# Kernel tuning notes

Measured on AMD Instinct MI355X. Metric: run time of the kernel, lower is better.

## Reference

```python
import jax, jax.numpy as jnp
import numpy as np

LEAKY_ALPHA = 0.2  # tf.nn.leaky_relu default

B, N, F_IN, HID = 1, 8192, 512, 256


def setup_inputs() -> dict:
    key = jax.random.key(0)
    ks = jax.random.split(key, 4)
    seq = jax.random.normal(ks[0], (B, N, F_IN), dtype=jnp.float32)
    bias_mat = jnp.zeros((B, N, N), dtype=jnp.float32)  # 0 = edge present (fully connected mask)
    W = jax.random.normal(ks[1], (F_IN, HID), dtype=jnp.float32) * (1.0 / np.sqrt(F_IN))
    a1 = jax.random.normal(ks[2], (HID, 1), dtype=jnp.float32) * (1.0 / np.sqrt(HID))
    b1 = jnp.zeros((1,), dtype=jnp.float32)
    a2 = jax.random.normal(ks[3], (HID, 1), dtype=jnp.float32) * (1.0 / np.sqrt(HID))
    b2 = jnp.zeros((1,), dtype=jnp.float32)
    bias_zero = jnp.zeros((HID,), dtype=jnp.float32)
    return {"seq": seq, "bias_mat": bias_mat, "W": W, "a1": a1, "b1": b1,
            "a2": a2, "b2": b2, "bias_zero": bias_zero}


def reference(seq, bias_mat, W, a1, b1, a2, b2, bias_zero):
    # Conv1D(kernel=1, no bias) == per-node linear projection
    seq_fts = jnp.einsum('bnf,fh->bnh', seq, W)            # [B,N,H]
    f_1 = jnp.einsum('bnh,ho->bno', seq_fts, a1) + b1      # [B,N,1]
    f_2 = jnp.einsum('bnh,ho->bno', seq_fts, a2) + b2      # [B,N,1]
    logits = f_1 + jnp.swapaxes(f_2, 1, 2)                 # [B,N,N] outer-sum
    scores = jnp.where(logits > 0, logits, LEAKY_ALPHA * logits) + bias_mat
    coefs = jax.nn.softmax(scores, axis=-1)                # masked softmax over neighbors
    vals = jnp.einsum('bnm,bmh->bnh', coefs, seq_fts)      # aggregation
    ret = vals + bias_zero
    return jax.nn.elu(ret)
```

## Files before the change

kernel.cpp:

```cpp
#include <hip/hip_runtime.h>
#include <hip/hip_bf16.h>
#include <stdint.h>

#define NN 8192
#define FIN 512
#define HID 256

typedef short bf16x8 __attribute__((ext_vector_type(8)));
typedef float f32x4 __attribute__((ext_vector_type(4)));

__device__ __forceinline__ uint32_t pk2(float lo, float hi) {
  uint32_t a = __float_as_uint(lo), b = __float_as_uint(hi);
  a = (a + 0x7FFFu + ((a >> 16) & 1u)) >> 16;
  b = (b + 0x7FFFu + ((b >> 16) & 1u)) >> 16;
  return a | (b << 16);
}

#define OFF_SEQB   0u
#define OFF_WTB    8388608u
#define OFF_FTST   8650752u
#define OFF_F1     12845056u
#define OFF_F2     12877824u
#define OFF_Z      12910592u
#define OFF_F2MAX  12943360u

__global__ void k_cvt_seq(const float* __restrict__ seq, short* __restrict__ seqb) {
  int i = (blockIdx.x * 256 + threadIdx.x) * 4;
  float4 v = *(const float4*)(seq + i);
  uint2 o; o.x = pk2(v.x, v.y); o.y = pk2(v.z, v.w);
  *(uint2*)(seqb + i) = o;
}

__global__ void k_wt(const float* __restrict__ W, short* __restrict__ WTb) {
  int h = blockIdx.x;
  int t = threadIdx.x;
  int k = t * 2;
  float w0 = W[k * 256 + h], w1 = W[(k + 1) * 256 + h];
  ((uint32_t*)(WTb + h * 512))[t] = pk2(w0, w1);
}

__global__ __launch_bounds__(256) void k_proj(
    const short* __restrict__ seqb, const short* __restrict__ WTb,
    const float* __restrict__ a1, const float* __restrict__ b1,
    const float* __restrict__ a2, const float* __restrict__ b2,
    short* __restrict__ ftsP, float* __restrict__ f1g, float* __restrict__ f2g,
    uint32_t* __restrict__ f2maxenc) {
  __shared__ short At[64][72];
  __shared__ float f1a[64], f2a[64];
  const int t = threadIdx.x;
  const int l = t & 63, w = t >> 6;
  const int lr = l & 15, lg = l >> 4;
  const int R0 = blockIdx.x * 64;
  const int srow = t >> 2, scol = (t & 3) * 16;
  f32x4 acc[4][4] = {};
  if (t < 64) { f1a[t] = 0.f; f2a[t] = 0.f; }
  for (int kt = 0; kt < FIN; kt += 64) {
    uint4 s0 = *(const uint4*)(seqb + (size_t)(R0 + srow) * FIN + kt + scol);
    uint4 s1 = *(const uint4*)(seqb + (size_t)(R0 + srow) * FIN + kt + scol + 8);
    __syncthreads();
    *(uint4*)&At[srow][scol] = s0;
    *(uint4*)&At[srow][scol + 8] = s1;
    __syncthreads();
#pragma unroll
    for (int kk = 0; kk < 2; ++kk) {
      bf16x8 af[4];
#pragma unroll
      for (int mf = 0; mf < 4; ++mf)
        af[mf] = *(const bf16x8*)&At[mf * 16 + lr][kk * 32 + lg * 8];
#pragma unroll
      for (int nf = 0; nf < 4; ++nf) {
        int h = w * 64 + nf * 16 + lr;
        bf16x8 bfr = *(const bf16x8*)(WTb + h * FIN + kt + kk * 32 + lg * 8);
#pragma unroll
        for (int mf = 0; mf < 4; ++mf)
          acc[mf][nf] = __builtin_amdgcn_mfma_f32_16x16x32_bf16(af[mf], bfr, acc[mf][nf], 0, 0, 0);
      }
    }
  }
  __syncthreads();
  float a1v[4], a2v[4];
#pragma unroll
  for (int nf = 0; nf < 4; ++nf) {
    int h = w * 64 + nf * 16 + lr;
    a1v[nf] = a1[h]; a2v[nf] = a2[h];
  }
#pragma unroll
  for (int mf = 0; mf < 4; ++mf) {
    const int jo = mf * 16 + lg * 4;
    const int slot = (jo >> 3) ^ (lr & 7);
#pragma unroll
    for (int nf = 0; nf < 4; ++nf) {
      int h = w * 64 + nf * 16 + lr;
      uint2 o; o.x = pk2(acc[mf][nf][0], acc[mf][nf][1]);
      o.y = pk2(acc[mf][nf][2], acc[mf][nf][3]);
      *(uint2*)(ftsP + (size_t)blockIdx.x * 16384 + h * 64 + slot * 8 + (jo & 7)) = o;
    }
#pragma unroll
    for (int e = 0; e < 4; ++e) {
      float p1 = 0.f, p2 = 0.f;
#pragma unroll
      for (int nf = 0; nf < 4; ++nf) { p1 += acc[mf][nf][e] * a1v[nf]; p2 += acc[mf][nf][e] * a2v[nf]; }
#pragma unroll
      for (int m = 8; m >= 1; m >>= 1) { p1 += __shfl_xor(p1, m, 16); p2 += __shfl_xor(p2, m, 16); }
      if (lr == 0) {
        atomicAdd(&f1a[mf * 16 + lg * 4 + e], p1);
        atomicAdd(&f2a[mf * 16 + lg * 4 + e], p2);
      }
    }
  }
  __syncthreads();
  if (t < 64) {
    float v1 = f1a[t] + b1[0];
    float v2 = f2a[t] + b2[0];
    f1g[R0 + t] = v1; f2g[R0 + t] = v2;
    uint32_t u = __float_as_uint(v2);
    u = (u & 0x80000000u) ? ~u : (u | 0x80000000u);
    atomicMax(f2maxenc, u);
  }
}

__global__ __launch_bounds__(512, 4) void k_flash(
    const float* __restrict__ bias, const short* __restrict__ ftsP,
    const float* __restrict__ f1g, const float* __restrict__ f2g,
    const uint32_t* __restrict__ f2maxenc,
    float* __restrict__ outacc, float* __restrict__ Zg) {
  __shared__ short Vb[2][16384];
  const int t = threadIdx.x;
  const int l = t & 63, wid = t >> 6;
  const int lr = l & 15, lg = l >> 4;
  const int hh = wid & 1;
  const int rg = wid >> 1;
  const int rbase = blockIdx.x * 64 + rg * 16;
  const int rowA = rbase + lr;
  const int jbase = blockIdx.y * 2048;
  const int jt0 = jbase >> 6;
  const int NT = 32;
  const int nfb = hh * 8;

  uint32_t ue = *f2maxenc;
  float f2mx = __uint_as_float((ue & 0x80000000u) ? (ue ^ 0x80000000u) : ~ue);
  float f1v = f1g[rowA];
  float xm = f1v + f2mx;
  float mr = fmaxf(xm, 0.2f * xm);

  const float* bp = bias + (size_t)rowA * NN + jbase + lg * 8;
  const float* qp = f2g + jbase + lg * 8;

  const int s0 = lg ^ (lr & 7);
  const int s1 = s0 ^ 4;

  f32x4 acc[8] = {};
  float z = 0.f;
  float4 bb[2][2], qq[2][2];

#define STAGE(TT, BUF)                                                          \
  if ((TT) < NT) {                                                              \
    const short* gs = ftsP + (size_t)(jt0 + (TT)) * 16384 + wid * 2048 + l * 8; \
    _Pragma("unroll")                                                           \
    for (int c = 0; c < 4; ++c)                                                 \
      __builtin_amdgcn_global_load_lds(                                         \
          (const __attribute__((address_space(1))) void*)(gs + c * 512),        \
          (__attribute__((address_space(3))) void*)&Vb[(BUF)][wid * 2048 + c * 512], \
          16, 0, 0);                                                            \
  }
#define LOADB(TT)                                                               \
  if ((TT) < NT) {                                                              \
    _Pragma("unroll")                                                           \
    for (int kk = 0; kk < 2; ++kk) {                                            \
      _Pragma("unroll")                                                         \
      for (int h4 = 0; h4 < 2; ++h4) {                                          \
        bb[kk][h4] = *(const float4*)(bp + (TT) * 64 + kk * 32 + h4 * 4);       \
        qq[kk][h4] = *(const float4*)(qp + (TT) * 64 + kk * 32 + h4 * 4);       \
      }                                                                         \
    }                                                                           \
  }
#define EHALF(BBK, QQK, AOUT)                                                   \
  {                                                                             \
    float p[8];                                                                 \
    _Pragma("unroll")                                                           \
    for (int e = 0; e < 4; ++e) {                                               \
      float s = f1v + ((const float*)&QQK[0])[e];                               \
      float ls = fmaxf(s, 0.2f * s);                                            \
      p[e] = __expf(ls + ((const float*)&BBK[0])[e] - mr);                      \
    }                                                                           \
    _Pragma("unroll")                                                           \
    for (int e = 0; e < 4; ++e) {                                               \
      float s = f1v + ((const float*)&QQK[1])[e];                               \
      float ls = fmaxf(s, 0.2f * s);                                            \
      p[4 + e] = __expf(ls + ((const float*)&BBK[1])[e] - mr);                  \
    }                                                                           \
    z += ((p[0] + p[1]) + (p[2] + p[3])) + ((p[4] + p[5]) + (p[6] + p[7]));     \
    union { bf16x8 v; uint32_t u[4]; } A;                                       \
    A.u[0] = pk2(p[0], p[1]); A.u[1] = pk2(p[2], p[3]);                         \
    A.u[2] = pk2(p[4], p[5]); A.u[3] = pk2(p[6], p[7]);                         \
    AOUT = A.v;                                                                 \
  }

  STAGE(0, 0)
  STAGE(1, 1)
  LOADB(0)
  __syncthreads();

  for (int tt = 0; tt < NT; ++tt) {
    bf16x8 A0, A1;
    EHALF(bb[0], qq[0], A0)
    EHALF(bb[1], qq[1], A1)

    LOADB(tt + 1)

    {
      const int cb = tt & 1;
      const short* vr0 = &Vb[cb][lr * 64 + s0 * 8];
      const short* vr1 = &Vb[cb][lr * 64 + s1 * 8];
#pragma unroll
      for (int nf = 0; nf < 8; ++nf) {
        bf16x8 B0 = *(const bf16x8*)(vr0 + (nfb + nf) * 1024);
        acc[nf] = __builtin_amdgcn_mfma_f32_16x16x32_bf16(A0, B0, acc[nf], 0, 0, 0);
      }
#pragma unroll
      for (int nf = 0; nf < 8; ++nf) {
        bf16x8 B1 = *(const bf16x8*)(vr1 + (nfb + nf) * 1024);
        acc[nf] = __builtin_amdgcn_mfma_f32_16x16x32_bf16(A1, B1, acc[nf], 0, 0, 0);
      }
    }

    __syncthreads();
    STAGE(tt + 2, tt & 1)
  }
#undef STAGE
#undef LOADB
#undef EHALF

  z += __shfl_xor(z, 16);
  z += __shfl_xor(z, 32);
  if (hh == 0 && lg == 0) atomicAdd(&Zg[rowA], z);

#pragma unroll
  for (int nf = 0; nf < 8; ++nf) {
    int col = (nfb + nf) * 16 + lr;
#pragma unroll
    for (int e = 0; e < 4; ++e)
      atomicAdd(&outacc[(size_t)(rbase + lg * 4 + e) * HID + col], acc[nf][e]);
  }
}

__global__ void k_final(float* __restrict__ outp, const float* __restrict__ Zg,
                        const float* __restrict__ bz) {
  int i4 = (blockIdx.x * 256 + threadIdx.x) * 4;
  int row = i4 >> 8;
  int col = i4 & 255;
  float4 v = *(float4*)(outp + i4);
  float zr = 1.0f / Zg[row];
  float4 b = *(const float4*)(bz + col);
  float r[4] = {v.x * zr + b.x, v.y * zr + b.y, v.z * zr + b.z, v.w * zr + b.w};
#pragma unroll
  for (int e = 0; e < 4; ++e) r[e] = r[e] > 0.f ? r[e] : (__expf(r[e]) - 1.f);
  *(float4*)(outp + i4) = make_float4(r[0], r[1], r[2], r[3]);
}

extern "C" void kernel_launch(void* const* d_in, const int* in_sizes, int n_in,
                              void* d_out, int out_size, void* d_ws, size_t ws_size,
                              hipStream_t stream) {
  const float* seq  = (const float*)d_in[0];
  const float* bias = (const float*)d_in[1];
  const float* W    = (const float*)d_in[2];
  const float* a1   = (const float*)d_in[3];
  const float* b1   = (const float*)d_in[4];
  const float* a2   = (const float*)d_in[5];
  const float* b2   = (const float*)d_in[6];
  const float* bz   = (const float*)d_in[7];
  float* out = (float*)d_out;
  char* ws = (char*)d_ws;
  short* seqb = (short*)(ws + OFF_SEQB);
  short* WTb  = (short*)(ws + OFF_WTB);
  short* ftsP = (short*)(ws + OFF_FTST);
  float* f1g  = (float*)(ws + OFF_F1);
  float* f2g  = (float*)(ws + OFF_F2);
  float* Zg   = (float*)(ws + OFF_Z);
  uint32_t* f2m = (uint32_t*)(ws + OFF_F2MAX);

  hipMemsetAsync(d_out, 0, (size_t)NN * HID * 4, stream);
  hipMemsetAsync(Zg, 0, NN * 4, stream);
  hipMemsetAsync(f2m, 0, 4, stream);

  k_cvt_seq<<<4096, 256, 0, stream>>>(seq, seqb);
  k_wt<<<256, 256, 0, stream>>>(W, WTb);
  k_proj<<<128, 256, 0, stream>>>(seqb, WTb, a1, b1, a2, b2, ftsP, f1g, f2g, f2m);
  k_flash<<<dim3(128, 4), 512, 0, stream>>>(bias, ftsP, f1g, f2g, f2m, out, Zg);
  k_final<<<2048, 256, 0, stream>>>(out, Zg, bz);
}
```

Baseline: 186.0 us.

## Give each flash wave all 256 output columns and prefetch bias four tiles ahead

The attention kernel shrinks from 8 to 4 waves per block. Each wave now owns 16 rows across all 256 hidden columns (16 accumulators), so the exp/leaky-relu probabilities are no longer computed twice by the two column-half waves. The bias-matrix loads are batched four tiles ahead with a manually unrolled loop to hide global latency, and staging copies 8 chunks per wave. The cost is doubled accumulator registers and lower occupancy per block, which may reduce latency hiding.

```diff
diff --git a/kernel.cpp b/kernel.cpp
--- a/kernel.cpp
+++ b/kernel.cpp
@@ -119,7 +119,7 @@
   }
 }
 
-__global__ __launch_bounds__(512, 4) void k_flash(
+__global__ __launch_bounds__(256, 2) void k_flash(
     const float* __restrict__ bias, const short* __restrict__ ftsP,
     const float* __restrict__ f1g, const float* __restrict__ f2g,
     const uint32_t* __restrict__ f2maxenc,
@@ -128,14 +128,11 @@
   const int t = threadIdx.x;
   const int l = t & 63, wid = t >> 6;
   const int lr = l & 15, lg = l >> 4;
-  const int hh = wid & 1;
-  const int rg = wid >> 1;
-  const int rbase = blockIdx.x * 64 + rg * 16;
+  const int rbase = blockIdx.x * 64 + wid * 16;
   const int rowA = rbase + lr;
   const int jbase = blockIdx.y * 2048;
   const int jt0 = jbase >> 6;
   const int NT = 32;
-  const int nfb = hh * 8;
 
   uint32_t ue = *f2maxenc;
   float f2mx = __uint_as_float((ue & 0x80000000u) ? (ue ^ 0x80000000u) : ~ue);
@@ -149,30 +146,35 @@
   const int s0 = lg ^ (lr & 7);
   const int s1 = s0 ^ 4;
 
-  f32x4 acc[8] = {};
+  f32x4 acc[16] = {};
   float z = 0.f;
-  float4 bb[2][2], qq[2][2];
+  float4 bbS0[2][2], bbS1[2][2], bbS2[2][2], bbS3[2][2];
+  float4 qq[2][2], nq[2][2];
 
 #define STAGE(TT, BUF)                                                          \
   if ((TT) < NT) {                                                              \
-    const short* gs = ftsP + (size_t)(jt0 + (TT)) * 16384 + wid * 2048 + l * 8; \
+    const short* gs = ftsP + (size_t)(jt0 + (TT)) * 16384 + wid * 4096 + l * 8; \
     _Pragma("unroll")                                                           \
-    for (int c = 0; c < 4; ++c)                                                 \
+    for (int c = 0; c < 8; ++c)                                                 \
       __builtin_amdgcn_global_load_lds(                                         \
           (const __attribute__((address_space(1))) void*)(gs + c * 512),        \
-          (__attribute__((address_space(3))) void*)&Vb[(BUF)][wid * 2048 + c * 512], \
+          (__attribute__((address_space(3))) void*)&Vb[(BUF)][wid * 4096 + c * 512], \
           16, 0, 0);                                                            \
   }
-#define LOADB(TT)                                                               \
+#define LB1(TT, B)                                                              \
   if ((TT) < NT) {                                                              \
-    _Pragma("unroll")                                                           \
-    for (int kk = 0; kk < 2; ++kk) {                                            \
-      _Pragma("unroll")                                                         \
-      for (int h4 = 0; h4 < 2; ++h4) {                                          \
-        bb[kk][h4] = *(const float4*)(bp + (TT) * 64 + kk * 32 + h4 * 4);       \
-        qq[kk][h4] = *(const float4*)(qp + (TT) * 64 + kk * 32 + h4 * 4);       \
-      }                                                                         \
-    }                                                                           \
+    B[0][0] = *(const float4*)(bp + (TT) * 64);                                 \
+    B[0][1] = *(const float4*)(bp + (TT) * 64 + 4);                             \
+    B[1][0] = *(const float4*)(bp + (TT) * 64 + 32);                            \
+    B[1][1] = *(const float4*)(bp + (TT) * 64 + 36);                            \
+  }
+#define LOADB4(T0) LB1((T0), bbS0) LB1((T0) + 1, bbS1) LB1((T0) + 2, bbS2) LB1((T0) + 3, bbS3)
+#define LOADF(TT, Q)                                                            \
+  if ((TT) < NT) {                                                              \
+    Q[0][0] = *(const float4*)(qp + (TT) * 64);                                 \
+    Q[0][1] = *(const float4*)(qp + (TT) * 64 + 4);                             \
+    Q[1][0] = *(const float4*)(qp + (TT) * 64 + 32);                            \
+    Q[1][1] = *(const float4*)(qp + (TT) * 64 + 36);                            \
   }
 #define EHALF(BBK, QQK, AOUT)                                                   \
   {                                                                             \
@@ -195,49 +197,62 @@
     A.u[2] = pk2(p[4], p[5]); A.u[3] = pk2(p[6], p[7]);                         \
     AOUT = A.v;                                                                 \
   }
+#define ITER(TT, SS, DO4)                                                       \
+  {                                                                             \
+    bf16x8 A0, A1;                                                              \
+    EHALF(SS[0], qq[0], A0)                                                     \
+    EHALF(SS[1], qq[1], A1)                                                     \
+    LOADF((TT) + 1, nq)                                                         \
+    if (DO4) { LOADB4((TT) + 1) }                                               \
+    {                                                                           \
+      const int cb = (TT) & 1;                                                  \
+      const short* vr0 = &Vb[cb][lr * 64 + s0 * 8];                             \
+      const short* vr1 = &Vb[cb][lr * 64 + s1 * 8];                             \
+      _Pragma("unroll")                                                         \
+      for (int nf = 0; nf < 16; ++nf) {                                         \
+        bf16x8 B0 = *(const bf16x8*)(vr0 + nf * 1024);                          \
+        acc[nf] = __builtin_amdgcn_mfma_f32_16x16x32_bf16(A0, B0, acc[nf], 0, 0, 0); \
+      }                                                                         \
+      _Pragma("unroll")                                                         \
+      for (int nf = 0; nf < 16; ++nf) {                                         \
+        bf16x8 B1 = *(const bf16x8*)(vr1 + nf * 1024);                          \
+        acc[nf] = __builtin_amdgcn_mfma_f32_16x16x32_bf16(A1, B1, acc[nf], 0, 0, 0); \
+      }                                                                         \
+    }                                                                           \
+    __syncthreads();                                                            \
+    STAGE((TT) + 2, (TT) & 1)                                                   \
+    _Pragma("unroll")                                                           \
+    for (int kk = 0; kk < 2; ++kk) {                                            \
+      qq[kk][0] = nq[kk][0]; qq[kk][1] = nq[kk][1];                             \
+    }                                                                           \
+  }
 
   STAGE(0, 0)
   STAGE(1, 1)
-  LOADB(0)
+  LOADB4(0)
+  LOADF(0, qq)
   __syncthreads();
 
-  for (int tt = 0; tt < NT; ++tt) {
-    bf16x8 A0, A1;
-    EHALF(bb[0], qq[0], A0)
-    EHALF(bb[1], qq[1], A1)
-
-    LOADB(tt + 1)
-
-    {
-      const int cb = tt & 1;
-      const short* vr0 = &Vb[cb][lr * 64 + s0 * 8];
-      const short* vr1 = &Vb[cb][lr * 64 + s1 * 8];
-#pragma unroll
-      for (int nf = 0; nf < 8; ++nf) {
-        bf16x8 B0 = *(const bf16x8*)(vr0 + (nfb + nf) * 1024);
-        acc[nf] = __builtin_amdgcn_mfma_f32_16x16x32_bf16(A0, B0, acc[nf], 0, 0, 0);
-      }
-#pragma unroll
-      for (int nf = 0; nf < 8; ++nf) {
-        bf16x8 B1 = *(const bf16x8*)(vr1 + (nfb + nf) * 1024);
-        acc[nf] = __builtin_amdgcn_mfma_f32_16x16x32_bf16(A1, B1, acc[nf], 0, 0, 0);
-      }
-    }
-
-    __syncthreads();
-    STAGE(tt + 2, tt & 1)
-  }
+  for (int tt = 0; tt < NT; tt += 4) {
+    ITER(tt, bbS0, 0)
+    ITER(tt + 1, bbS1, 0)
+    ITER(tt + 2, bbS2, 0)
+    ITER(tt + 3, bbS3, 1)
+  }
+#undef ITER
+#undef EHALF
+#undef LOADF
+#undef LOADB4
+#undef LB1
 #undef STAGE
-#undef LOADB
-#undef EHALF
 
   z += __shfl_xor(z, 16);
   z += __shfl_xor(z, 32);
-  if (hh == 0 && lg == 0) atomicAdd(&Zg[rowA], z);
-
-#pragma unroll
-  for (int nf = 0; nf < 8; ++nf) {
-    int col = (nfb + nf) * 16 + lr;
+  if (lg == 0) atomicAdd(&Zg[rowA], z);
+
+#pragma unroll
+  for (int nf = 0; nf < 16; ++nf) {
+    int col = nf * 16 + lr;
 #pragma unroll
     for (int e = 0; e < 4; ++e)
       atomicAdd(&outacc[(size_t)(rbase + lg * 4 + e) * HID + col], acc[nf][e]);
@@ -286,6 +301,6 @@
   k_cvt_seq<<<4096, 256, 0, stream>>>(seq, seqb);
   k_wt<<<256, 256, 0, stream>>>(W, WTb);
   k_proj<<<128, 256, 0, stream>>>(seqb, WTb, a1, b1, a2, b2, ftsP, f1g, f2g, f2m);
-  k_flash<<<dim3(128, 4), 512, 0, stream>>>(bias, ftsP, f1g, f2g, f2m, out, Zg);
+  k_flash<<<dim3(128, 4), 256, 0, stream>>>(bias, ftsP, f1g, f2g, f2m, out, Zg);
   k_final<<<2048, 256, 0, stream>>>(out, Zg, bz);
 }
```

Result: faster. 174.0 us (-6.5%).
